# Kernel tuning notes

Measured on AMD Instinct MI355X. Metric: run time of the kernel, lower is better.

The kernel has to match this reference:

```python
import jax, jax.numpy as jnp
import numpy as np

EPS = 1e-5

def _bn_relu_over_batch(x, gamma, beta):
    # x: [..., B, F] where batch axis is -2; per-step training-mode BatchNorm1d
    mu = x.mean(axis=-2, keepdims=True)
    var = ((x - mu) ** 2).mean(axis=-2, keepdims=True)  # biased var (torch BN)
    xn = (x - mu) * jax.lax.rsqrt(var + EPS)
    return jax.nn.relu(xn * gamma + beta)

def setup_inputs() -> dict:
    key = jax.random.key(0)
    ks = jax.random.split(key, 8)
    B, T, D_in, E, C, D_out = 8192, 128, 2, 128, 128, 5
    s = 0.1
    return {
        "inputs": jax.random.normal(ks[0], (B, T, D_in), jnp.float32),
        "W_emb": jax.random.normal(ks[1], (E, D_in), jnp.float32) * s,
        "b_emb": jnp.zeros((E,), jnp.float32),
        "g_emb": jnp.ones((E,), jnp.float32),
        "be_emb": jnp.zeros((E,), jnp.float32),
        "W_ih": jax.random.normal(ks[2], (4 * C, E), jnp.float32) * s,
        "W_hh": jax.random.normal(ks[3], (4 * C, C), jnp.float32) * s,
        "b_ih": jnp.zeros((4 * C,), jnp.float32),
        "b_hh": jnp.zeros((4 * C,), jnp.float32),
        "W_out": jax.random.normal(ks[4], (D_out, C), jnp.float32) * s,
        "b_out": jnp.zeros((D_out,), jnp.float32),
        "g_out": jnp.ones((D_out,), jnp.float32),
        "be_out": jnp.zeros((D_out,), jnp.float32),
    }

def reference(inputs, W_emb, b_emb, g_emb, be_emb, W_ih, W_hh, b_ih, b_hh,
              W_out, b_out, g_out, be_out):
    B, T, _ = inputs.shape
    C = W_hh.shape[1]
    # Input embedding: Linear + per-step BatchNorm (batch stats) + ReLU, vectorized over T
    x = jnp.einsum('btd,ed->bte', inputs, W_emb) + b_emb      # [B,T,E]
    x = jnp.transpose(x, (1, 0, 2))                           # [T,B,E]
    x = _bn_relu_over_batch(x, g_emb, be_emb)                 # BN over batch per step

    def step(carry, xt):
        h, c = carry
        gates = xt @ W_ih.T + b_ih + h @ W_hh.T + b_hh        # [B,4C]
        i, f, g, o = jnp.split(gates, 4, axis=-1)             # torch LSTMCell order
        i = jax.nn.sigmoid(i); f = jax.nn.sigmoid(f)
        g = jnp.tanh(g); o = jax.nn.sigmoid(o)
        c = f * c + i * g
        h = o * jnp.tanh(c)
        return (h, c), h

    h0 = jnp.zeros((B, C), inputs.dtype)
    _, h_all = jax.lax.scan(step, (h0, h0), x)                # [T,B,C]

    # Output embedding: Linear + per-step BatchNorm + ReLU
    y = jnp.einsum('tbc,oc->tbo', h_all, W_out) + b_out       # [T,B,5]
    y = _bn_relu_over_batch(y, g_out, be_out)
    return jnp.transpose(y, (1, 0, 2))                        # [B,T,5]
```

## Files before the change

### kernel.cpp

```cpp
#include <hip/hip_runtime.h>

typedef __attribute__((ext_vector_type(8))) short short8;
typedef __attribute__((ext_vector_type(4))) float floatx4;

#define B_TOT 8192
#define T_STEPS 128
#define E_DIM 128
#define C_DIM 128
#define D_OUT 5
#define BN_EPS 1e-5f

#define LOG2E 1.4426950408889634f
#define TWO_LOG2E 2.8853900817779268f

#define WS_WCAT   0u
#define WS_WOUT   (WS_WCAT + 262144u)
#define WS_A0     (WS_WOUT + 4096u)
#define WS_A1     (WS_A0 + 65536u)
#define WS_CC     (WS_A1 + 65536u)
#define WS_STATS  (WS_CC + 65536u)
#define WS_PART   (WS_STATS + 5120u)
#define WS_Y      (WS_PART + 20480u)

__device__ __forceinline__ float bf2f(unsigned short h){
  return __uint_as_float(((unsigned int)h) << 16);
}
__device__ __forceinline__ unsigned short f2b(float v){
  unsigned int u = __float_as_uint(v);
  u += 0x7FFFu + ((u >> 16) & 1u);
  return (unsigned short)(u >> 16);
}
__device__ __forceinline__ unsigned short f2b_fast(float v){
  return (unsigned short)((__float_as_uint(v) + 0x8000u) >> 16);
}
__device__ __forceinline__ float ldf(const void* p, int i, int bf){
  return bf ? bf2f(((const unsigned short*)p)[i]) : ((const float*)p)[i];
}
__device__ __forceinline__ int sniff_bf(const void* ones){
  return *(const unsigned int*)ones == 0x3F803F80u;
}

__global__ void k_prep_mom(const void* W_ih, const void* W_hh, const void* W_out,
                           unsigned short* wcat, unsigned short* wout,
                           const void* x, float* part, const void* ones){
  const int bf = sniff_bf(ones);
  const int tid = threadIdx.x;
  if (blockIdx.x < 260){
    int i = blockIdx.x * 512 + tid;
    if (i < 512*256){
      int n = i >> 8, k = i & 255;
      float v = (k < 128) ? ldf(W_ih, n*128 + k, bf) : ldf(W_hh, n*128 + (k-128), bf);
      float sc = ((n >> 7) == 2) ? TWO_LOG2E : -LOG2E;
      wcat[i] = f2b(v * sc);
    } else {
      int j = i - 512*256;
      int n = j >> 7, k = j & 127;
      float v = (n < D_OUT) ? ldf(W_out, n*128 + k, bf) : 0.0f;
      wout[j] = f2b(v);
    }
    return;
  }
  const int mb  = blockIdx.x - 260;
  const int wdw = (mb >> 3) * 8;
  const int rg  = mb & 7;
  const int wv = tid >> 6, lane = tid & 63;
  __shared__ float red[8][16][3];

  if (!bf){
    const float* xp = (const float*)x;
    const int row_b = tid >> 4, j = tid & 15;
    float a0=0, a1=0, a2=0;
    for (int c = 0; c < 32; ++c){
      int row = rg*1024 + c*32 + row_b;
      float v = xp[row*256 + wdw*2 + j];
      float p = __shfl_xor(v, 1, 64);
      if ((j & 1) == 0){ a0 += v; a1 += v*v; a2 += v*p; }
      else             { a0 += v; a1 += v*v; }
    }
    a0 += __shfl_down(a0,32,64); a0 += __shfl_down(a0,16,64);
    a1 += __shfl_down(a1,32,64); a1 += __shfl_down(a1,16,64);
    a2 += __shfl_down(a2,32,64); a2 += __shfl_down(a2,16,64);
    if (lane < 16){ red[wv][lane][0]=a0; red[wv][lane][1]=a1; red[wv][lane][2]=a2; }
  } else {
    const unsigned int* xp = (const unsigned int*)x;
    const int row_b = tid >> 3, j = tid & 7;
    float s0=0,s1=0,s00=0,s11=0,s01=0;
    for (int c = 0; c < 16; ++c){
      int row = rg*1024 + c*64 + row_b;
      unsigned int u = xp[row*128 + wdw + j];
      float xv0 = bf2f((unsigned short)(u & 0xFFFFu));
      float xv1 = bf2f((unsigned short)(u >> 16));
      s0+=xv0; s1+=xv1; s00+=xv0*xv0; s11+=xv1*xv1; s01+=xv0*xv1;
    }
    s0 += __shfl_down(s0,32,64); s0 += __shfl_down(s0,16,64); s0 += __shfl_down(s0,8,64);
    s1 += __shfl_down(s1,32,64); s1 += __shfl_down(s1,16,64); s1 += __shfl_down(s1,8,64);
    s00+= __shfl_down(s00,32,64);s00+= __shfl_down(s00,16,64);s00+= __shfl_down(s00,8,64);
    s11+= __shfl_down(s11,32,64);s11+= __shfl_down(s11,16,64);s11+= __shfl_down(s11,8,64);
    s01+= __shfl_down(s01,32,64);s01+= __shfl_down(s01,16,64);s01+= __shfl_down(s01,8,64);
    if (lane < 8){
      red[wv][lane][0]=s0;  red[wv][lane][1]=s00; red[wv][lane][2]=s01;
      red[wv][8+lane][0]=s1; red[wv][8+lane][1]=s11;
    }
  }
  __syncthreads();
  if (tid < 8){
    int tl = tid;
    float S0=0,S1=0,S00=0,S11=0,S01=0;
    for (int w8 = 0; w8 < 8; ++w8){
      if (!bf){
        S0 += red[w8][2*tl][0];   S00 += red[w8][2*tl][1];   S01 += red[w8][2*tl][2];
        S1 += red[w8][2*tl+1][0]; S11 += red[w8][2*tl+1][1];
      } else {
        S0 += red[w8][tl][0];     S00 += red[w8][tl][1];     S01 += red[w8][tl][2];
        S1 += red[w8][8+tl][0];   S11 += red[w8][8+tl][1];
      }
    }
    float* dst = part + rg*640 + (wdw + tl)*5;
    dst[0]=S0; dst[1]=S1; dst[2]=S00; dst[3]=S11; dst[4]=S01;
  }
}

__global__ void k_coef(const float* part, const void* W_emb, const void* g_emb, const void* be_emb,
                       float* A0, float* A1, float* Cc){
  const int bf = sniff_bf(g_emb);
  int i = blockIdx.x*256 + threadIdx.x;
  int t = i >> 7, e = i & 127;
  float S0=0,S1=0,S00=0,S11=0,S01=0;
  for (int rg = 0; rg < 8; ++rg){
    const float* p = part + rg*640 + t*5;
    S0+=p[0]; S1+=p[1]; S00+=p[2]; S11+=p[3]; S01+=p[4];
  }
  const float inv = 1.0f / (float)B_TOT;
  float mu0 = S0*inv, mu1 = S1*inv;
  float v00 = S00*inv - mu0*mu0, v11 = S11*inv - mu1*mu1, c01 = S01*inv - mu0*mu1;
  float w0 = ldf(W_emb, e*2, bf), w1 = ldf(W_emb, e*2+1, bf);
  float g  = ldf(g_emb, e, bf),  be = ldf(be_emb, e, bf);
  float var = w0*w0*v00 + 2.0f*w0*w1*c01 + w1*w1*v11;
  float rs = rsqrtf(var + BN_EPS);
  float a0 = g*rs*w0, a1 = g*rs*w1;
  A0[i] = a0; A1[i] = a1;
  Cc[i] = be - (a0*mu0 + a1*mu1);
}

__global__ __launch_bounds__(512, 2)
void k_lstm(const void* x, const void* b_ih, const void* b_hh, const void* ones,
            const unsigned short* __restrict__ wcat, const unsigned short* __restrict__ wout,
            const float* __restrict__ A0, const float* __restrict__ A1, const float* __restrict__ Cc,
            float* __restrict__ y_ws){
  const int bf = sniff_bf(ones);
  const int tid = threadIdx.x;
  const int wid = tid >> 6, lane = tid & 63;
  const int q = lane >> 4, s = lane & 15;
  const int row0 = blockIdx.x * 32;

  __shared__ unsigned short xh[2][32][264];

  {
    short8 z;
#pragma unroll
    for (int j = 0; j < 8; ++j) z[j] = 0;
    unsigned short* base = &xh[0][0][0];
    for (int i = tid*8; i < 2*32*264; i += 512*8)
      *(short8*)(base + i) = z;
  }

  short8 bfr[4][8];
#pragma unroll
  for (int gq = 0; gq < 4; ++gq)
#pragma unroll
    for (int ks = 0; ks < 8; ++ks)
      bfr[gq][ks] = *(const short8*)(wcat + ((wid + 8*gq)*16 + s)*256 + ks*32 + q*8);

  short8 wf[4];
#pragma unroll
  for (int ks = 0; ks < 4; ++ks)
    wf[ks] = *(const short8*)(wout + s*128 + ks*32 + q*8);

  const int ch = 16*wid + s;
  floatx4 binit[4];
#pragma unroll
  for (int gq = 0; gq < 4; ++gq){
    float braw = ldf(b_ih, gq*128 + ch, bf) + ldf(b_hh, gq*128 + ch, bf);
    float b = braw * ((gq == 2) ? TWO_LOG2E : -LOG2E);
    binit[gq] = (floatx4){b, b, b, b};
  }

  float c_st[2][4] = {{0,0,0,0},{0,0,0,0}};

  const int r_loc = tid >> 4;
  const int e0 = (tid & 15) * 8;

  auto compute_xe = [&](int tt, int buf){
    float x0, x1;
    int xbase = ((row0 + r_loc)*T_STEPS + tt)*2;
    if (bf){ const unsigned short* xp = (const unsigned short*)x;
      x0 = bf2f(xp[xbase]); x1 = bf2f(xp[xbase+1]);
    } else { const float* xp = (const float*)x; x0 = xp[xbase]; x1 = xp[xbase+1]; }
    floatx4 a0a = *(const floatx4*)(A0 + tt*E_DIM + e0);
    floatx4 a0b = *(const floatx4*)(A0 + tt*E_DIM + e0 + 4);
    floatx4 a1a = *(const floatx4*)(A1 + tt*E_DIM + e0);
    floatx4 a1b = *(const floatx4*)(A1 + tt*E_DIM + e0 + 4);
    floatx4 cca = *(const floatx4*)(Cc + tt*E_DIM + e0);
    floatx4 ccb = *(const floatx4*)(Cc + tt*E_DIM + e0 + 4);
    short8 pack;
#pragma unroll
    for (int j = 0; j < 4; ++j){
      float v  = fmaxf(fmaf(a0a[j], x0, fmaf(a1a[j], x1, cca[j])), 0.0f);
      float v2 = fmaxf(fmaf(a0b[j], x0, fmaf(a1b[j], x1, ccb[j])), 0.0f);
      pack[j]   = (short)f2b_fast(v);
      pack[4+j] = (short)f2b_fast(v2);
    }
    *(short8*)&xh[buf][r_loc][e0] = pack;
  };

  __syncthreads();
  compute_xe(0, 0);
  __syncthreads();

  for (int t = 0; t < T_STEPS; ++t){
    const int cb = t & 1, nb = cb ^ 1;

    if (wid < 2 && t > 0){
      floatx4 ya = {0,0,0,0};
#pragma unroll
      for (int ks = 0; ks < 4; ++ks){
        short8 a = *(const short8*)&xh[cb][s + 16*wid][128 + ks*32 + q*8];
        ya = __builtin_amdgcn_mfma_f32_16x16x32_bf16(a, wf[ks], ya, 0, 0, 0);
      }
      if (s < D_OUT){
#pragma unroll
        for (int r = 0; r < 4; ++r){
          int row = row0 + 16*wid + q*4 + r;
          y_ws[((t-1)*B_TOT + row)*D_OUT + s] = ya[r];
        }
      }
    }

    floatx4 acc[2][4];
#pragma unroll
    for (int mt = 0; mt < 2; ++mt)
#pragma unroll
      for (int gq = 0; gq < 4; ++gq) acc[mt][gq] = binit[gq];
#pragma unroll
    for (int ks = 0; ks < 8; ++ks){
      short8 a0 = *(const short8*)&xh[cb][s][ks*32 + q*8];
      short8 a1 = *(const short8*)&xh[cb][s + 16][ks*32 + q*8];
#pragma unroll
      for (int gq = 0; gq < 4; ++gq){
        acc[0][gq] = __builtin_amdgcn_mfma_f32_16x16x32_bf16(a0, bfr[gq][ks], acc[0][gq], 0, 0, 0);
        acc[1][gq] = __builtin_amdgcn_mfma_f32_16x16x32_bf16(a1, bfr[gq][ks], acc[1][gq], 0, 0, 0);
      }
    }

#pragma unroll
    for (int mt = 0; mt < 2; ++mt){
#pragma unroll
      for (int r = 0; r < 4; ++r){
        float ea = __builtin_amdgcn_exp2f(fminf(acc[mt][0][r], 40.0f));
        float eb = __builtin_amdgcn_exp2f(fminf(acc[mt][1][r], 40.0f));
        float ec = __builtin_amdgcn_exp2f(fminf(acc[mt][2][r], 40.0f));
        float ed = __builtin_amdgcn_exp2f(fminf(acc[mt][3][r], 40.0f));
        float Aa = 1.0f + ea, Bb = 1.0f + eb, Ca = 1.0f + ec;
        float t1 = Aa * Ca;
        float r1 = __builtin_amdgcn_rcpf(t1 * Bb);
        float cn = fmaf(t1 * r1, c_st[mt][r], (Bb * r1) * (ec - 1.0f));
        c_st[mt][r] = cn;
        float E  = __builtin_amdgcn_exp2f(fminf(cn * TWO_LOG2E, 80.0f));
        float r2 = __builtin_amdgcn_rcpf((1.0f + ed) * (E + 1.0f));
        float hv = (E - 1.0f) * r2;
        xh[nb][16*mt + q*4 + r][128 + ch] = f2b_fast(hv);
      }
    }

    if (t < T_STEPS-1) compute_xe(t+1, nb);
    __syncthreads();
  }

  if (wid < 2){
    floatx4 ya = {0,0,0,0};
#pragma unroll
    for (int ks = 0; ks < 4; ++ks){
      short8 a = *(const short8*)&xh[0][s + 16*wid][128 + ks*32 + q*8];
      ya = __builtin_amdgcn_mfma_f32_16x16x32_bf16(a, wf[ks], ya, 0, 0, 0);
    }
    if (s < D_OUT){
#pragma unroll
      for (int r = 0; r < 4; ++r){
        int row = row0 + 16*wid + q*4 + r;
        y_ws[((T_STEPS-1)*B_TOT + row)*D_OUT + s] = ya[r];
      }
    }
  }
  asm volatile("s_waitcnt vmcnt(0)" ::: "memory");
}

__global__ void k_outstats(const float* __restrict__ y_ws, const void* g_out, const void* be_out,
                           float* stats, const void* ones){
  const int bf = sniff_bf(ones);
  const int t = blockIdx.x, tid = threadIdx.x;
  __shared__ float acc2[5][2];
  if (tid < 10) ((float*)acc2)[tid] = 0.0f;
  __syncthreads();
  float s[5] = {0,0,0,0,0}, ss[5] = {0,0,0,0,0};
  const float* base = y_ws + (size_t)t * 40960;
#pragma unroll 5
  for (int it = 0; it < 160; ++it){
    float v = base[it*256 + tid];
    s[it % 5] += v; ss[it % 5] += v*v;
  }
  int ob = tid % 5;
#pragma unroll
  for (int p = 0; p < 5; ++p){
    int o = ob + p; if (o >= 5) o -= 5;
    atomicAdd(&acc2[o][0], s[p]);
    atomicAdd(&acc2[o][1], ss[p]);
  }
  __syncthreads();
  if (tid < 5){
    float S = acc2[tid][0], SS = acc2[tid][1];
    const float inv = 1.0f / (float)B_TOT;
    float mu = S*inv, var = SS*inv - mu*mu;
    float g = ldf(g_out, tid, bf), be = ldf(be_out, tid, bf);
    float sc = g * rsqrtf(var + BN_EPS);
    stats[(t*5+tid)*2]   = sc;
    stats[(t*5+tid)*2+1] = be - sc*mu;
  }
}

__global__ void k_apply(const float* __restrict__ y_ws, const float* __restrict__ stats,
                        void* out, const void* ones){
  const int bf = sniff_bf(ones);
  __shared__ float tile[128*85];
  const int b0 = blockIdx.x * 16;
  const int tid = threadIdx.x;
  for (int i = tid; i < 10240; i += 256){
    int t = i / 80, j = i - t*80;
    tile[t*85 + j] = y_ws[((size_t)t*B_TOT + b0)*D_OUT + j];
  }
  __syncthreads();
  for (int i = tid; i < 10240; i += 256){
    int b = i / 640, r = i - b*640;
    int t = r / 5, o = r - t*5;
    float v = tile[t*85 + b*5 + o];
    v = fmaxf(fmaf(v, stats[r*2], stats[r*2+1]), 0.0f);
    int oi = b0*640 + i;
    if (bf) ((unsigned short*)out)[oi] = f2b(v);
    else    ((float*)out)[oi] = v;
  }
}

extern "C" void kernel_launch(void* const* d_in, const int* in_sizes, int n_in,
                              void* d_out, int out_size, void* d_ws, size_t ws_size,
                              hipStream_t stream){
  const void* x      = d_in[0];
  const void* W_emb  = d_in[1];
  const void* g_emb  = d_in[3];
  const void* be_emb = d_in[4];
  const void* W_ih   = d_in[5];
  const void* W_hh   = d_in[6];
  const void* b_ih   = d_in[7];
  const void* b_hh   = d_in[8];
  const void* W_out  = d_in[9];
  const void* g_out  = d_in[11];
  const void* be_out = d_in[12];

  char* ws = (char*)d_ws;
  unsigned short* wcat = (unsigned short*)(ws + WS_WCAT);
  unsigned short* wout = (unsigned short*)(ws + WS_WOUT);
  float* A0    = (float*)(ws + WS_A0);
  float* A1    = (float*)(ws + WS_A1);
  float* Cc    = (float*)(ws + WS_CC);
  float* stats = (float*)(ws + WS_STATS);
  float* part  = (float*)(ws + WS_PART);
  float* y_ws  = (float*)(ws + WS_Y);

  k_prep_mom<<<dim3(388),  dim3(512), 0, stream>>>(W_ih, W_hh, W_out, wcat, wout, x, part, g_emb);
  k_coef    <<<dim3(64),   dim3(256), 0, stream>>>(part, W_emb, g_emb, be_emb, A0, A1, Cc);
  k_lstm    <<<dim3(256),  dim3(512), 0, stream>>>(x, b_ih, b_hh, g_emb, wcat, wout, A0, A1, Cc, y_ws);
  k_outstats<<<dim3(128),  dim3(256), 0, stream>>>(y_ws, g_out, be_out, stats, g_emb);
  k_apply   <<<dim3(512),  dim3(256), 0, stream>>>(y_ws, stats, d_out, g_emb);
}
```

Measured before the change: 427.7 us.

## Halve LSTM block batch tile to 16 rows and launch twice as many blocks

Each LSTM block now handles 16 batch rows instead of 32, with 512 blocks instead of 256 and a launch-bounds occupancy hint raised to 4 blocks. Each wave does one M-tile of MFMAs per gate per step instead of two, so the serial per-step chain in a block gets shorter and work spreads across more CUs. The cost is that every block reloads the full recurrent weight set into registers. The weights are also reused over half as many rows, and the higher occupancy target may force register spilling of the 32 short8 weight fragments.

```diff
diff --git a/kernel.cpp b/kernel.cpp
--- a/kernel.cpp
+++ b/kernel.cpp
@@ -1,6 +1,7 @@
 #include <hip/hip_runtime.h>
 
 typedef __attribute__((ext_vector_type(8))) short short8;
+typedef __attribute__((ext_vector_type(4))) short short4v;
 typedef __attribute__((ext_vector_type(4))) float floatx4;
 
 #define B_TOT 8192
@@ -142,7 +143,7 @@
   Cc[i] = be - (a0*mu0 + a1*mu1);
 }
 
-__global__ __launch_bounds__(512, 2)
+__global__ __launch_bounds__(512, 4)
 void k_lstm(const void* x, const void* b_ih, const void* b_hh, const void* ones,
             const unsigned short* __restrict__ wcat, const unsigned short* __restrict__ wout,
             const float* __restrict__ A0, const float* __restrict__ A1, const float* __restrict__ Cc,
@@ -151,16 +152,16 @@
   const int tid = threadIdx.x;
   const int wid = tid >> 6, lane = tid & 63;
   const int q = lane >> 4, s = lane & 15;
-  const int row0 = blockIdx.x * 32;
-
-  __shared__ unsigned short xh[2][32][264];
+  const int row0 = blockIdx.x * 16;
+
+  __shared__ unsigned short xh[2][16][264];
 
   {
     short8 z;
 #pragma unroll
     for (int j = 0; j < 8; ++j) z[j] = 0;
     unsigned short* base = &xh[0][0][0];
-    for (int i = tid*8; i < 2*32*264; i += 512*8)
+    for (int i = tid*8; i < 2*16*264; i += 512*8)
       *(short8*)(base + i) = z;
   }
 
@@ -177,18 +178,17 @@
     wf[ks] = *(const short8*)(wout + s*128 + ks*32 + q*8);
 
   const int ch = 16*wid + s;
-  floatx4 binit[4];
+  float binit[4];
 #pragma unroll
   for (int gq = 0; gq < 4; ++gq){
     float braw = ldf(b_ih, gq*128 + ch, bf) + ldf(b_hh, gq*128 + ch, bf);
-    float b = braw * ((gq == 2) ? TWO_LOG2E : -LOG2E);
-    binit[gq] = (floatx4){b, b, b, b};
-  }
-
-  float c_st[2][4] = {{0,0,0,0},{0,0,0,0}};
-
-  const int r_loc = tid >> 4;
-  const int e0 = (tid & 15) * 8;
+    binit[gq] = braw * ((gq == 2) ? TWO_LOG2E : -LOG2E);
+  }
+
+  float c_st[4] = {0,0,0,0};
+
+  const int r_loc = tid >> 5;
+  const int e0 = (tid & 31) * 4;
 
   auto compute_xe = [&](int tt, int buf){
     float x0, x1;
@@ -197,20 +197,15 @@
       x0 = bf2f(xp[xbase]); x1 = bf2f(xp[xbase+1]);
     } else { const float* xp = (const float*)x; x0 = xp[xbase]; x1 = xp[xbase+1]; }
     floatx4 a0a = *(const floatx4*)(A0 + tt*E_DIM + e0);
-    floatx4 a0b = *(const floatx4*)(A0 + tt*E_DIM + e0 + 4);
     floatx4 a1a = *(const floatx4*)(A1 + tt*E_DIM + e0);
-    floatx4 a1b = *(const floatx4*)(A1 + tt*E_DIM + e0 + 4);
     floatx4 cca = *(const floatx4*)(Cc + tt*E_DIM + e0);
-    floatx4 ccb = *(const floatx4*)(Cc + tt*E_DIM + e0 + 4);
-    short8 pack;
+    short4v pack;
 #pragma unroll
     for (int j = 0; j < 4; ++j){
-      float v  = fmaxf(fmaf(a0a[j], x0, fmaf(a1a[j], x1, cca[j])), 0.0f);
-      float v2 = fmaxf(fmaf(a0b[j], x0, fmaf(a1b[j], x1, ccb[j])), 0.0f);
-      pack[j]   = (short)f2b_fast(v);
-      pack[4+j] = (short)f2b_fast(v2);
-    }
-    *(short8*)&xh[buf][r_loc][e0] = pack;
+      float v = fmaxf(fmaf(a0a[j], x0, fmaf(a1a[j], x1, cca[j])), 0.0f);
+      pack[j] = (short)f2b_fast(v);
+    }
+    *(short4v*)&xh[buf][r_loc][e0] = pack;
   };
 
   __syncthreads();
@@ -220,73 +215,66 @@
   for (int t = 0; t < T_STEPS; ++t){
     const int cb = t & 1, nb = cb ^ 1;
 
-    if (wid < 2 && t > 0){
+    if (wid == 0 && t > 0){
       floatx4 ya = {0,0,0,0};
 #pragma unroll
       for (int ks = 0; ks < 4; ++ks){
-        short8 a = *(const short8*)&xh[cb][s + 16*wid][128 + ks*32 + q*8];
+        short8 a = *(const short8*)&xh[cb][s][128 + ks*32 + q*8];
         ya = __builtin_amdgcn_mfma_f32_16x16x32_bf16(a, wf[ks], ya, 0, 0, 0);
       }
       if (s < D_OUT){
 #pragma unroll
         for (int r = 0; r < 4; ++r){
-          int row = row0 + 16*wid + q*4 + r;
+          int row = row0 + q*4 + r;
           y_ws[((t-1)*B_TOT + row)*D_OUT + s] = ya[r];
         }
       }
     }
 
-    floatx4 acc[2][4];
-#pragma unroll
-    for (int mt = 0; mt < 2; ++mt)
-#pragma unroll
-      for (int gq = 0; gq < 4; ++gq) acc[mt][gq] = binit[gq];
+    floatx4 acc[4];
+#pragma unroll
+    for (int gq = 0; gq < 4; ++gq)
+      acc[gq] = (floatx4){binit[gq], binit[gq], binit[gq], binit[gq]};
 #pragma unroll
     for (int ks = 0; ks < 8; ++ks){
       short8 a0 = *(const short8*)&xh[cb][s][ks*32 + q*8];
-      short8 a1 = *(const short8*)&xh[cb][s + 16][ks*32 + q*8];
-#pragma unroll
-      for (int gq = 0; gq < 4; ++gq){
-        acc[0][gq] = __builtin_amdgcn_mfma_f32_16x16x32_bf16(a0, bfr[gq][ks], acc[0][gq], 0, 0, 0);
-        acc[1][gq] = __builtin_amdgcn_mfma_f32_16x16x32_bf16(a1, bfr[gq][ks], acc[1][gq], 0, 0, 0);
-      }
-    }
-
-#pragma unroll
-    for (int mt = 0; mt < 2; ++mt){
-#pragma unroll
-      for (int r = 0; r < 4; ++r){
-        float ea = __builtin_amdgcn_exp2f(fminf(acc[mt][0][r], 40.0f));
-        float eb = __builtin_amdgcn_exp2f(fminf(acc[mt][1][r], 40.0f));
-        float ec = __builtin_amdgcn_exp2f(fminf(acc[mt][2][r], 40.0f));
-        float ed = __builtin_amdgcn_exp2f(fminf(acc[mt][3][r], 40.0f));
-        float Aa = 1.0f + ea, Bb = 1.0f + eb, Ca = 1.0f + ec;
-        float t1 = Aa * Ca;
-        float r1 = __builtin_amdgcn_rcpf(t1 * Bb);
-        float cn = fmaf(t1 * r1, c_st[mt][r], (Bb * r1) * (ec - 1.0f));
-        c_st[mt][r] = cn;
-        float E  = __builtin_amdgcn_exp2f(fminf(cn * TWO_LOG2E, 80.0f));
-        float r2 = __builtin_amdgcn_rcpf((1.0f + ed) * (E + 1.0f));
-        float hv = (E - 1.0f) * r2;
-        xh[nb][16*mt + q*4 + r][128 + ch] = f2b_fast(hv);
-      }
+#pragma unroll
+      for (int gq = 0; gq < 4; ++gq)
+        acc[gq] = __builtin_amdgcn_mfma_f32_16x16x32_bf16(a0, bfr[gq][ks], acc[gq], 0, 0, 0);
+    }
+
+#pragma unroll
+    for (int r = 0; r < 4; ++r){
+      float ea = __builtin_amdgcn_exp2f(fminf(acc[0][r], 40.0f));
+      float eb = __builtin_amdgcn_exp2f(fminf(acc[1][r], 40.0f));
+      float ec = __builtin_amdgcn_exp2f(fminf(acc[2][r], 40.0f));
+      float ed = __builtin_amdgcn_exp2f(fminf(acc[3][r], 40.0f));
+      float Aa = 1.0f + ea, Bb = 1.0f + eb, Ca = 1.0f + ec;
+      float t1 = Aa * Ca;
+      float r1 = __builtin_amdgcn_rcpf(t1 * Bb);
+      float cn = fmaf(t1 * r1, c_st[r], (Bb * r1) * (ec - 1.0f));
+      c_st[r] = cn;
+      float E  = __builtin_amdgcn_exp2f(fminf(cn * TWO_LOG2E, 80.0f));
+      float r2 = __builtin_amdgcn_rcpf((1.0f + ed) * (E + 1.0f));
+      float hv = (E - 1.0f) * r2;
+      xh[nb][q*4 + r][128 + ch] = f2b_fast(hv);
     }
 
     if (t < T_STEPS-1) compute_xe(t+1, nb);
     __syncthreads();
   }
 
-  if (wid < 2){
+  if (wid == 0){
     floatx4 ya = {0,0,0,0};
 #pragma unroll
     for (int ks = 0; ks < 4; ++ks){
-      short8 a = *(const short8*)&xh[0][s + 16*wid][128 + ks*32 + q*8];
+      short8 a = *(const short8*)&xh[0][s][128 + ks*32 + q*8];
       ya = __builtin_amdgcn_mfma_f32_16x16x32_bf16(a, wf[ks], ya, 0, 0, 0);
     }
     if (s < D_OUT){
 #pragma unroll
       for (int r = 0; r < 4; ++r){
-        int row = row0 + 16*wid + q*4 + r;
+        int row = row0 + q*4 + r;
         y_ws[((T_STEPS-1)*B_TOT + row)*D_OUT + s] = ya[r];
       }
     }
@@ -376,7 +364,7 @@
 
   k_prep_mom<<<dim3(388),  dim3(512), 0, stream>>>(W_ih, W_hh, W_out, wcat, wout, x, part, g_emb);
   k_coef    <<<dim3(64),   dim3(256), 0, stream>>>(part, W_emb, g_emb, be_emb, A0, A1, Cc);
-  k_lstm    <<<dim3(256),  dim3(512), 0, stream>>>(x, b_ih, b_hh, g_emb, wcat, wout, A0, A1, Cc, y_ws);
+  k_lstm    <<<dim3(512),  dim3(512), 0, stream>>>(x, b_ih, b_hh, g_emb, wcat, wout, A0, A1, Cc, y_ws);
   k_outstats<<<dim3(128),  dim3(256), 0, stream>>>(y_ws, g_out, be_out, stats, g_emb);
   k_apply   <<<dim3(512),  dim3(256), 0, stream>>>(y_ws, stats, d_out, g_emb);
 }
```

Result: slower. 1.277 ms (+198.6%).
